# Optimization experiments

Hardware: AMD Instinct MI355X
Metric: run time of the kernel (lower is better)

## Reference

```python
import jax, jax.numpy as jnp
import numpy as np

N_COMP = 48
RES = 300
N_FEAT = 27
N_PTS = 1_000_000


def _sample_plane(plane, gx, gy):
    # plane: [C, H, W]; gx, gy: [N] grid coords in [-1, 1]; bilinear, align_corners=True
    C, H, W = plane.shape
    x = (gx + 1.0) * 0.5 * (W - 1)
    y = (gy + 1.0) * 0.5 * (H - 1)
    x0f = jnp.floor(x)
    y0f = jnp.floor(y)
    wx = x - x0f
    wy = y - y0f
    x0 = jnp.clip(x0f, 0, W - 1).astype(jnp.int32)
    y0 = jnp.clip(y0f, 0, H - 1).astype(jnp.int32)
    x1 = jnp.clip(x0 + 1, 0, W - 1)
    y1 = jnp.clip(y0 + 1, 0, H - 1)
    v00 = plane[:, y0, x0]  # [C, N]
    v01 = plane[:, y0, x1]
    v10 = plane[:, y1, x0]
    v11 = plane[:, y1, x1]
    return (1.0 - wy) * ((1.0 - wx) * v00 + wx * v01) + wy * ((1.0 - wx) * v10 + wx * v11)


def _sample_line(line, gy):
    # line: [C, R] (width dim of size 1 squeezed; grid x == 0 -> column 0); gy: [N]
    C, R = line.shape
    y = (gy + 1.0) * 0.5 * (R - 1)
    y0f = jnp.floor(y)
    wy = y - y0f
    y0 = jnp.clip(y0f, 0, R - 1).astype(jnp.int32)
    y1 = jnp.clip(y0 + 1, 0, R - 1)
    return (1.0 - wy) * line[:, y0] + wy * line[:, y1]  # [C, N]


def setup_inputs():
    key = jax.random.key(0)
    k0, k1, k2, k3 = jax.random.split(key, 4)
    xyz = jax.random.uniform(k0, (N_PTS, 3), jnp.float32) * 2.0 - 1.0
    planes = 0.1 * jax.random.uniform(k1, (3, N_COMP, RES, RES), jnp.float32)
    lines = 0.1 * jax.random.uniform(k2, (3, N_COMP, RES, 1), jnp.float32)
    basis_W = jax.random.normal(k3, (N_FEAT, 3 * N_COMP), jnp.float32) / jnp.sqrt(3.0 * N_COMP)
    return {"xyz_sampled": xyz, "planes": planes, "lines": lines, "basis_W": basis_W}


def reference(xyz_sampled, planes, lines, basis_W):
    # plane i samples (x=xyz[:,a], y=xyz[:,b]) with (a,b) per torch's xyz[..., [2,1]/[2,0]/[1,0]]
    PLANE_AX = ((2, 1), (2, 0), (1, 0))
    pf, lf = [], []
    for i in range(3):
        a, b = PLANE_AX[i]
        pf.append(_sample_plane(planes[i], xyz_sampled[:, a], xyz_sampled[:, b]))
        lf.append(_sample_line(lines[i, :, :, 0], xyz_sampled[:, i]))
    pf = jnp.concatenate(pf, axis=0)  # [3C, N]
    lf = jnp.concatenate(lf, axis=0)  # [3C, N]
    # basis_mat: Linear(3C -> n_features, bias=False) applied to (pf*lf).T
    return (pf * lf).T @ basis_W.T  # [N, n_features]
```

## Files before the change

kernel.cpp:

```cpp
#include <hip/hip_runtime.h>

namespace {

constexpr int NCOMP = 48;
constexpr int RESN  = 300;
constexpr int NFEAT = 27;
constexpr int NPTS  = 1000000;
constexpr int CCTOT = 3 * NCOMP;
constexpr int GRID1 = 32;
constexpr int NBUCKET = GRID1 * GRID1 * GRID1;

typedef _Float16 half_t;
typedef __attribute__((ext_vector_type(8))) _Float16 half8;
typedef __attribute__((ext_vector_type(2))) _Float16 half2_t;
typedef __attribute__((ext_vector_type(8))) short          short8;
typedef __attribute__((ext_vector_type(4))) unsigned int   uint4_t;
typedef __attribute__((ext_vector_type(4))) float          floatx4;

__device__ __forceinline__ unsigned short f32_to_bf16(float x) {
    unsigned u = __float_as_uint(x);
    u += 0x7fffu + ((u >> 16) & 1u);
    return (unsigned short)(u >> 16);
}

__device__ __forceinline__ half2_t bc_h2(float x) {
    union { float f; half2_t h; } u; u.f = x; return u.h;
}
__device__ __forceinline__ float h2_bc(half2_t h) {
    union { float f; half2_t h; } u; u.h = h; return u.f;
}

constexpr int SH_STRIDE = 48;

constexpr int LT_PAD = 64;

constexpr int TP_TOTAL  = 3 * RESN * RESN;
constexpr int TP_BLOCKS = (TP_TOTAL + 255) / 256;
constexpr int LINES_TOT = 3 * RESN;
constexpr int WT_TOT    = NFEAT * CCTOT;
constexpr int WFRAG_TOT = 3 * 2 * 2 * 64 * 8;
constexpr int SU_TOTAL  = LINES_TOT + WT_TOT + WFRAG_TOT + LT_PAD;
constexpr int SU_BLOCKS = (SU_TOTAL + 255) / 256;
constexpr int HB_BLOCKS = (NPTS + 255) / 256;

__device__ __forceinline__ int cell_of(float q) {
    float t = (q + 1.0f) * (0.5f * (float)GRID1);
    int c = (int)t;
    return min(max(c, 0), GRID1 - 1);
}
__device__ __forceinline__ int key_of(float q0, float q1, float q2) {
    return (cell_of(q0) * GRID1 + cell_of(q1)) * GRID1 + cell_of(q2);
}

__global__ __launch_bounds__(256) void fused_front_k(
    const float* __restrict__ planes, const float* __restrict__ lines,
    const float* __restrict__ W, const float* __restrict__ xyz,
    half_t* __restrict__ pt, half_t* __restrict__ lt,
    float* __restrict__ wt, unsigned short* __restrict__ wfrag,
    int* __restrict__ hist) {
    int b = blockIdx.x;
    if (b < TP_BLOCKS) {
        int idx = b * 256 + threadIdx.x;
        if (idx >= TP_TOTAL) return;
        int i   = idx / (RESN * RESN);
        int rem = idx - i * (RESN * RESN);
        const float* s = planes + (size_t)i * NCOMP * RESN * RESN + rem;
        half8* d = (half8*)(pt + (size_t)idx * NCOMP);
#pragma unroll
        for (int g = 0; g < NCOMP / 8; ++g) {
            half8 h;
#pragma unroll
            for (int k = 0; k < 8; ++k)
                h[k] = (half_t)s[(size_t)(g * 8 + k) * (RESN * RESN)];
            d[g] = h;
        }
        return;
    }
    if (b < TP_BLOCKS + SU_BLOCKS) {
        int idx = (b - TP_BLOCKS) * 256 + threadIdx.x;
        if (idx < LINES_TOT) {
            int i = idx / RESN;
            int y = idx - i * RESN;
            const float* s = lines + (size_t)i * NCOMP * RESN + y;
            half8* d = (half8*)(lt + (size_t)idx * NCOMP);
#pragma unroll
            for (int g = 0; g < NCOMP / 8; ++g) {
                half8 h;
#pragma unroll
                for (int k = 0; k < 8; ++k)
                    h[k] = (half_t)s[(size_t)(g * 8 + k) * RESN];
                d[g] = h;
            }
            return;
        }
        idx -= LINES_TOT;
        if (idx < WT_TOT) {
            int f  = idx / CCTOT;
            int cc = idx - f * CCTOT;
            wt[(size_t)cc * NFEAT + f] = W[idx];
            return;
        }
        idx -= WT_TOT;
        if (idx < WFRAG_TOT) {
            int j    = idx & 7;
            int lane = (idx >> 3) & 63;
            int nn   = (idx >> 9) & 1;
            int kb   = (idx >> 10) & 1;
            int md   = idx >> 11;
            int f  = nn * 16 + (lane & 15);
            int kk = kb * 32 + ((lane >> 4) << 3) + j;
            float vf = 0.0f;
            if (f < NFEAT && kk < NCOMP)
                vf = W[(size_t)f * CCTOT + md * NCOMP + kk];
            wfrag[idx] = f32_to_bf16(vf);
            return;
        }
        idx -= WFRAG_TOT;
        if (idx < LT_PAD) lt[(size_t)3 * RESN * NCOMP + idx] = (half_t)0.f;
        return;
    }
    int p = (b - TP_BLOCKS - SU_BLOCKS) * 256 + threadIdx.x;
    if (p >= NPTS || !hist) return;
    float q0 = xyz[3 * (size_t)p + 0];
    float q1 = xyz[3 * (size_t)p + 1];
    float q2 = xyz[3 * (size_t)p + 2];
    atomicAdd(&hist[key_of(q0, q1, q2)], 1);
}


__global__ __launch_bounds__(1024) void scan_k(const int* __restrict__ hist,
                                               int* __restrict__ start) {
    __shared__ int part[1024];
    int t = threadIdx.x;
    int base = t * (NBUCKET / 1024);
    int s = 0;
#pragma unroll 4
    for (int j = 0; j < NBUCKET / 1024; ++j) s += hist[base + j];
    part[t] = s;
    __syncthreads();
    for (int off = 1; off < 1024; off <<= 1) {
        int v = (t >= off) ? part[t - off] : 0;
        __syncthreads();
        part[t] += v;
        __syncthreads();
    }
    int run = (t == 0) ? 0 : part[t - 1];
    for (int j = 0; j < NBUCKET / 1024; ++j) {
        start[base + j] = run;
        run += hist[base + j];
    }
}

__global__ __launch_bounds__(256) void scatter_k(const float* __restrict__ xyz,
                                                 int* __restrict__ start,
                                                 float4* __restrict__ xyzs) {
    int p = blockIdx.x * blockDim.x + threadIdx.x;
    if (p >= NPTS) return;
    float q0 = xyz[3 * (size_t)p + 0];
    float q1 = xyz[3 * (size_t)p + 1];
    float q2 = xyz[3 * (size_t)p + 2];
    int slot = atomicAdd(&start[key_of(q0, q1, q2)], 1);
    float4 v;
    v.x = q0; v.y = q1; v.z = q2; v.w = __int_as_float(p);
    xyzs[slot] = v;
}


__device__ __forceinline__ void mfma_phase(const unsigned short* __restrict__ shw,
                                           int r, int q,
                                           short8 blo0, short8 blo1,
                                           short8 bhi0, short8 bhi1,
                                           floatx4 acc[4][2]) {
    const short8 z8 = {0, 0, 0, 0, 0, 0, 0, 0};
#pragma unroll
    for (int m = 0; m < 4; ++m) {
        const unsigned short* rb = shw + (size_t)(m * 16 + r) * SH_STRIDE;
        short8 alo = *(const short8*)(rb + q * 8);
        short8 ahl = *(const short8*)(rb + 32 + (q & 1) * 8);
        short8 ahi = (q < 2) ? ahl : z8;
        acc[m][0] = __builtin_amdgcn_mfma_f32_16x16x32_bf16(alo, blo0, acc[m][0], 0, 0, 0);
        acc[m][0] = __builtin_amdgcn_mfma_f32_16x16x32_bf16(ahi, bhi0, acc[m][0], 0, 0, 0);
        acc[m][1] = __builtin_amdgcn_mfma_f32_16x16x32_bf16(alo, blo1, acc[m][1], 0, 0, 0);
        acc[m][1] = __builtin_amdgcn_mfma_f32_16x16x32_bf16(ahi, bhi1, acc[m][1], 0, 0, 0);
    }
}

constexpr int MAIN_BLK = 128;
constexpr int MAIN_NWG = (NPTS + MAIN_BLK - 1) / MAIN_BLK;

__device__ __forceinline__ int swz_main(int orig) {
    constexpr int Q = MAIN_NWG / 8, R = MAIN_NWG % 8;
    int x = orig & 7, p = orig >> 3;
    return (x < R ? x * (Q + 1) : R * (Q + 1) + (x - R) * Q) + p;
}

__global__ __launch_bounds__(MAIN_BLK, 4) void tensor_vm_mfma_kernel(
    const float4* __restrict__ xyzs,
    const half_t* __restrict__ pt,
    const half_t* __restrict__ lt,
    const unsigned short* __restrict__ wfrag,
    float* __restrict__ out) {
    __shared__ unsigned short sh[2][64][SH_STRIDE];
    __shared__ float          sp[2][64][8];

    const int bid = swz_main(blockIdx.x);
    const int tid = threadIdx.x;
    const int w  = tid >> 6;
    const int ln = tid & 63;
    const int r  = ln & 15;
    const int q  = ln >> 4;
    const int gidx = bid * MAIN_BLK + tid;
    const int i = min(gidx, NPTS - 1);
    float4 v = xyzs[i];
    const int permInt = __float_as_int(v.w);

    floatx4 acc[4][2];
    const floatx4 z = {0.f, 0.f, 0.f, 0.f};
#pragma unroll
    for (int m = 0; m < 4; ++m) { acc[m][0] = z; acc[m][1] = z; }

    constexpr size_t PSZ = (size_t)RESN * RESN * NCOMP;
    constexpr size_t LSZ = (size_t)RESN * NCOMP;

    const unsigned short* shw = &sh[w][0][0];

    const float gxs[3] = {v.z, v.z, v.y};
    const float gys[3] = {v.y, v.x, v.x};
    const float gls[3] = {v.x, v.y, v.z};

#pragma unroll
    for (int md = 0; md < 3; ++md) {
        const unsigned short* wfb = wfrag + (size_t)md * 2048 + (size_t)ln * 8;
        short8 blo0 = *(const short8*)(wfb);
        short8 blo1 = *(const short8*)(wfb + 512);
        short8 bhi0 = *(const short8*)(wfb + 1024);
        short8 bhi1 = *(const short8*)(wfb + 1536);

        {
            float x = (gxs[md] + 1.0f) * 0.5f * (float)(RESN - 1);
            float y = (gys[md] + 1.0f) * 0.5f * (float)(RESN - 1);
            float l = (gls[md] + 1.0f) * 0.5f * (float)(RESN - 1);
            float x0f = floorf(x), y0f = floorf(y), l0f = floorf(l);
            float wx = x - x0f, wy = y - y0f, wl = l - l0f;
            int x0 = max(0, min((int)x0f, RESN - 1));
            int y0 = max(0, min((int)y0f, RESN - 1));
            int l0 = max(0, min((int)l0f, RESN - 1));
            int y1 = min(y0 + 1, RESN - 1);
            int off0 = (y0 * RESN + x0) * NCOMP * 2;
            int off1 = (y1 * RESN + x0) * NCOMP * 2;
            int offL = l0 * NCOMP * 2;
            half_t hx = (half_t)wx, hy = (half_t)wy, hl = (half_t)wl;
            half2_t wx2 = {hx, hx}, wy2 = {hy, hy}, wl2 = {hl, hl};
            float4 A, B;
            A.x = __int_as_float(off0); A.y = __int_as_float(off1);
            A.z = __int_as_float(offL); A.w = h2_bc(wx2);
            B.x = h2_bc(wy2); B.y = h2_bc(wl2); B.z = 0.f; B.w = 0.f;
            *(float4*)&sp[w][ln][0] = A;
            *(float4*)&sp[w][ln][4] = B;
        }
        __builtin_amdgcn_sched_barrier(0);

        const char* pmd = (const char*)(pt + md * PSZ);
        const char* lmd = (const char*)(lt + md * LSZ);
#pragma unroll
        for (int it = 0; it < 6; ++it) {
            unsigned pair = (unsigned)(it * 64 + ln);
            unsigned p = (pair * 10923u) >> 16;
            unsigned s = pair - p * 6u;
            float4 A = *(const float4*)&sp[w][p][0];
            float4 B = *(const float4*)&sp[w][p][4];
            int off0 = __float_as_int(A.x);
            int off1 = __float_as_int(A.y);
            int offL = __float_as_int(A.z);
            half2_t wx2 = bc_h2(A.w), wy2 = bc_h2(B.x), wl2 = bc_h2(B.y);
            int so = (int)(s * 16u);
            union H8 { half8 v; half2_t h2[4]; } a, b, c, d, e, f;
            a.v = *(const half8*)(pmd + off0 + so);
            b.v = *(const half8*)(pmd + off0 + 96 + so);
            c.v = *(const half8*)(pmd + off1 + so);
            d.v = *(const half8*)(pmd + off1 + 96 + so);
            e.v = *(const half8*)(lmd + offL + so);
            f.v = *(const half8*)(lmd + offL + 96 + so);
            uint4_t ho;
#pragma unroll
            for (int k = 0; k < 4; ++k) {
                half2_t pa = a.h2[k], pb = b.h2[k], pc = c.h2[k], pd = d.h2[k];
                half2_t px0 = pa + wx2 * (pb - pa);
                half2_t px1 = pc + wx2 * (pd - pc);
                half2_t pv  = px0 + wy2 * (px1 - px0);
                half2_t lv  = e.h2[k] + wl2 * (f.h2[k] - e.h2[k]);
                half2_t pr  = pv * lv;
                float f0 = (float)pr[0], f1 = (float)pr[1];
                unsigned o;
                asm("v_cvt_pk_bf16_f32 %0, %1, %2" : "=v"(o) : "v"(f0), "v"(f1));
                ho[k] = o;
            }
            *(uint4_t*)(&sh[w][p][s * 8u]) = ho;
        }

        asm volatile("s_waitcnt lgkmcnt(0)" ::: "memory");
        __builtin_amdgcn_sched_barrier(0);
        mfma_phase(shw, r, q, blo0, blo1, bhi0, bhi1, acc);
        __builtin_amdgcn_sched_barrier(0);
    }

    const int blockBase = bid * MAIN_BLK + w * 64;
#pragma unroll
    for (int m = 0; m < 4; ++m) {
#pragma unroll
        for (int rr = 0; rr < 4; ++rr) {
            const int pl = m * 16 + q * 4 + rr;
            const int pp = __shfl(permInt, pl);
            if (blockBase + pl < NPTS) {
                float* o = out + (size_t)pp * NFEAT + r;
                o[0] = acc[m][0][rr];
                if (r < NFEAT - 16) o[16] = acc[m][1][rr];
            }
        }
    }
}


__device__ __forceinline__ void accum_mode(float gx, float gy, float gl,
                                           const half_t* __restrict__ pt_i,
                                           const half_t* __restrict__ lt_i,
                                           const float* __restrict__ wt_i,
                                           float* __restrict__ acc) {
    float x = (gx + 1.0f) * 0.5f * (float)(RESN - 1);
    float y = (gy + 1.0f) * 0.5f * (float)(RESN - 1);
    float l = (gl + 1.0f) * 0.5f * (float)(RESN - 1);
    float x0f = floorf(x), y0f = floorf(y), l0f = floorf(l);
    float wx = x - x0f, wy = y - y0f, wl = l - l0f;
    int x0 = (int)x0f; x0 = max(0, min(x0, RESN - 1));
    int y0 = (int)y0f; y0 = max(0, min(y0, RESN - 1));
    int l0 = (int)l0f; l0 = max(0, min(l0, RESN - 1));
    int x1 = min(x0 + 1, RESN - 1);
    int y1 = min(y0 + 1, RESN - 1);
    int l1 = min(l0 + 1, RESN - 1);
    float w00 = (1.0f - wy) * (1.0f - wx);
    float w01 = (1.0f - wy) * wx;
    float w10 = wy * (1.0f - wx);
    float w11 = wy * wx;
    float wl0 = 1.0f - wl;
    float wl1 = wl;
    const half8* p00 = (const half8*)(pt_i + ((size_t)y0 * RESN + x0) * NCOMP);
    const half8* p01 = (const half8*)(pt_i + ((size_t)y0 * RESN + x1) * NCOMP);
    const half8* p10 = (const half8*)(pt_i + ((size_t)y1 * RESN + x0) * NCOMP);
    const half8* p11 = (const half8*)(pt_i + ((size_t)y1 * RESN + x1) * NCOMP);
    const half8* L0  = (const half8*)(lt_i + (size_t)l0 * NCOMP);
    const half8* L1  = (const half8*)(lt_i + (size_t)l1 * NCOMP);
#pragma unroll 2
    for (int g = 0; g < NCOMP / 8; ++g) {
        half8 a = p00[g], b = p01[g], c = p10[g], d = p11[g];
        half8 e0 = L0[g], e1 = L1[g];
#pragma unroll
        for (int j = 0; j < 8; ++j) {
            float pv = w00 * (float)a[j] + w01 * (float)b[j]
                     + w10 * (float)c[j] + w11 * (float)d[j];
            float lv = wl0 * (float)e0[j] + wl1 * (float)e1[j];
            float pr = pv * lv;
            const float* wrow = wt_i + (size_t)(8 * g + j) * NFEAT;
#pragma unroll
            for (int f = 0; f < NFEAT; ++f)
                acc[f] += pr * wrow[f];
        }
    }
}

__global__ __launch_bounds__(256) void tensor_vm_kernel(
    const float* __restrict__ xyz,
    const half_t* __restrict__ pt,
    const half_t* __restrict__ lt,
    const float* __restrict__ wt,
    float* __restrict__ out) {
    int p = blockIdx.x * blockDim.x + threadIdx.x;
    if (p >= NPTS) return;
    float q0 = xyz[3 * (size_t)p + 0];
    float q1 = xyz[3 * (size_t)p + 1];
    float q2 = xyz[3 * (size_t)p + 2];
    float acc[NFEAT];
#pragma unroll
    for (int f = 0; f < NFEAT; ++f) acc[f] = 0.0f;
    constexpr size_t PSZ = (size_t)RESN * RESN * NCOMP;
    constexpr size_t LSZ = (size_t)RESN * NCOMP;
    constexpr int    WSZ = NCOMP * NFEAT;
    accum_mode(q2, q1, q0, pt,           lt,           wt,           acc);
    accum_mode(q2, q0, q1, pt + PSZ,     lt + LSZ,     wt + WSZ,     acc);
    accum_mode(q1, q0, q2, pt + 2 * PSZ, lt + 2 * LSZ, wt + 2 * WSZ, acc);
    float* o = out + (size_t)p * NFEAT;
#pragma unroll
    for (int f = 0; f < NFEAT; ++f) o[f] = acc[f];
}

__global__ __launch_bounds__(256) void tensor_vm_naive_kernel(
    const float* __restrict__ xyz,
    const float* __restrict__ planes,
    const float* __restrict__ lines,
    const float* __restrict__ W,
    float* __restrict__ out) {
    int p = blockIdx.x * blockDim.x + threadIdx.x;
    if (p >= NPTS) return;
    float q[3];
    q[0] = xyz[3 * (size_t)p + 0];
    q[1] = xyz[3 * (size_t)p + 1];
    q[2] = xyz[3 * (size_t)p + 2];
    float acc[NFEAT];
    for (int f = 0; f < NFEAT; ++f) acc[f] = 0.0f;
    const int AX[3] = {2, 2, 1};
    const int BX[3] = {1, 0, 0};
    for (int i = 0; i < 3; ++i) {
        float gx = q[AX[i]], gy = q[BX[i]], gl = q[i];
        float x = (gx + 1.0f) * 0.5f * (float)(RESN - 1);
        float y = (gy + 1.0f) * 0.5f * (float)(RESN - 1);
        float l = (gl + 1.0f) * 0.5f * (float)(RESN - 1);
        float x0f = floorf(x), y0f = floorf(y), l0f = floorf(l);
        float wx = x - x0f, wy = y - y0f, wl = l - l0f;
        int x0 = max(0, min((int)x0f, RESN - 1));
        int y0 = max(0, min((int)y0f, RESN - 1));
        int l0 = max(0, min((int)l0f, RESN - 1));
        int x1 = min(x0 + 1, RESN - 1);
        int y1 = min(y0 + 1, RESN - 1);
        int l1 = min(l0 + 1, RESN - 1);
        float w00 = (1.0f - wy) * (1.0f - wx);
        float w01 = (1.0f - wy) * wx;
        float w10 = wy * (1.0f - wx);
        float w11 = wy * wx;
        const float* pl = planes + (size_t)i * NCOMP * RESN * RESN;
        const float* ln = lines + (size_t)i * NCOMP * RESN;
        for (int c = 0; c < NCOMP; ++c) {
            const float* plc = pl + (size_t)c * RESN * RESN;
            float v00 = plc[(size_t)y0 * RESN + x0];
            float v01 = plc[(size_t)y0 * RESN + x1];
            float v10 = plc[(size_t)y1 * RESN + x0];
            float v11 = plc[(size_t)y1 * RESN + x1];
            float pv = w00 * v00 + w01 * v01 + w10 * v10 + w11 * v11;
            float lv = (1.0f - wl) * ln[(size_t)c * RESN + l0] + wl * ln[(size_t)c * RESN + l1];
            float pr = pv * lv;
            int cc = i * NCOMP + c;
            for (int f = 0; f < NFEAT; ++f)
                acc[f] += pr * W[(size_t)f * CCTOT + cc];
        }
    }
    float* o = out + (size_t)p * NFEAT;
    for (int f = 0; f < NFEAT; ++f) o[f] = acc[f];
}

}

extern "C" void kernel_launch(void* const* d_in, const int* in_sizes, int n_in,
                              void* d_out, int out_size, void* d_ws, size_t ws_size,
                              hipStream_t stream) {
    (void)in_sizes; (void)n_in; (void)out_size;
    const float* xyz    = (const float*)d_in[0];
    const float* planes = (const float*)d_in[1];
    const float* lines  = (const float*)d_in[2];
    const float* W      = (const float*)d_in[3];
    float* out = (float*)d_out;

    constexpr size_t PT_HALVES   = (size_t)3 * RESN * RESN * NCOMP;
    constexpr size_t LT_HALVES   = (size_t)3 * RESN * NCOMP + LT_PAD;
    constexpr size_t WT_FLOATS   = (size_t)CCTOT * NFEAT;

    constexpr size_t WT_BYTES    = WT_FLOATS * sizeof(float);
    constexpr size_t WFRAG_BYTES = (size_t)WFRAG_TOT * 2;
    constexpr size_t PT_BYTES    = PT_HALVES * sizeof(half_t);
    constexpr size_t LT_BYTES    = LT_HALVES * sizeof(half_t);
    constexpr size_t HIST_BYTES  = (size_t)NBUCKET * sizeof(int);
    constexpr size_t XYZS_BYTES  = (size_t)NPTS * sizeof(float4);
    constexpr size_t NEED_PLAIN  = WT_BYTES + WFRAG_BYTES + PT_BYTES + LT_BYTES;
    constexpr size_t NEED_SORT   = NEED_PLAIN + 2 * HIST_BYTES + XYZS_BYTES;

    if (ws_size >= NEED_PLAIN) {
        float*          wt    = (float*)d_ws;
        unsigned short* wfrag = (unsigned short*)((char*)d_ws + WT_BYTES);
        half_t*         pt    = (half_t*)((char*)d_ws + WT_BYTES + WFRAG_BYTES);
        half_t*         lt    = (half_t*)((char*)d_ws + WT_BYTES + WFRAG_BYTES + PT_BYTES);
        if (ws_size >= NEED_SORT) {
            int*    hist  = (int*)((char*)d_ws + NEED_PLAIN);
            int*    start = (int*)((char*)d_ws + NEED_PLAIN + HIST_BYTES);
            float4* xyzs  = (float4*)((char*)d_ws + NEED_PLAIN + 2 * HIST_BYTES);
            hipMemsetAsync(hist, 0, HIST_BYTES, stream);
            fused_front_k<<<TP_BLOCKS + SU_BLOCKS + HB_BLOCKS, 256, 0, stream>>>(
                planes, lines, W, xyz, pt, lt, wt, wfrag, hist);
            scan_k<<<1, 1024, 0, stream>>>(hist, start);
            scatter_k<<<(NPTS + 255) / 256, 256, 0, stream>>>(xyz, start, xyzs);
            tensor_vm_mfma_kernel<<<MAIN_NWG, MAIN_BLK, 0, stream>>>(
                xyzs, pt, lt, wfrag, out);
        } else {
            fused_front_k<<<TP_BLOCKS + SU_BLOCKS, 256, 0, stream>>>(
                planes, lines, W, xyz, pt, lt, wt, wfrag, nullptr);
            tensor_vm_kernel<<<(NPTS + 255) / 256, 256, 0, stream>>>(xyz, pt, lt, wt, out);
        }
    } else {
        tensor_vm_naive_kernel<<<(NPTS + 255) / 256, 256, 0, stream>>>(xyz, planes, lines, W, out);
    }
}
```

Baseline: 401.8 us.

## Drop spatial bucket sort and XCD swizzle; read xyz directly in MFMA kernel

Removes the histogram, scan and scatter passes that sorted points into 32^3 spatial buckets, along with the XCD-aware block swizzle. The MFMA kernel now reads the raw xyz input in original order and writes output rows directly, with no permutation shuffle. This saves the memset, the atomics, a single-block scan and an extra pass over the points. The cost is that, with uniformly random points, neighbouring threads gather from scattered plane texels, so cache locality on the roughly 26 MB fp16 plane table is lost.

Measured after the change: 359.6 us. 1.12x faster.

```diff
diff --git a/kernel.cpp b/kernel.cpp
--- a/kernel.cpp
+++ b/kernel.cpp
@@ -7,8 +7,6 @@
 constexpr int NFEAT = 27;
 constexpr int NPTS  = 1000000;
 constexpr int CCTOT = 3 * NCOMP;
-constexpr int GRID1 = 32;
-constexpr int NBUCKET = GRID1 * GRID1 * GRID1;
 
 typedef _Float16 half_t;
 typedef __attribute__((ext_vector_type(8))) _Float16 half8;
@@ -41,23 +39,12 @@
 constexpr int WFRAG_TOT = 3 * 2 * 2 * 64 * 8;
 constexpr int SU_TOTAL  = LINES_TOT + WT_TOT + WFRAG_TOT + LT_PAD;
 constexpr int SU_BLOCKS = (SU_TOTAL + 255) / 256;
-constexpr int HB_BLOCKS = (NPTS + 255) / 256;
-
-__device__ __forceinline__ int cell_of(float q) {
-    float t = (q + 1.0f) * (0.5f * (float)GRID1);
-    int c = (int)t;
-    return min(max(c, 0), GRID1 - 1);
-}
-__device__ __forceinline__ int key_of(float q0, float q1, float q2) {
-    return (cell_of(q0) * GRID1 + cell_of(q1)) * GRID1 + cell_of(q2);
-}
 
 __global__ __launch_bounds__(256) void fused_front_k(
     const float* __restrict__ planes, const float* __restrict__ lines,
-    const float* __restrict__ W, const float* __restrict__ xyz,
+    const float* __restrict__ W,
     half_t* __restrict__ pt, half_t* __restrict__ lt,
-    float* __restrict__ wt, unsigned short* __restrict__ wfrag,
-    int* __restrict__ hist) {
+    float* __restrict__ wt, unsigned short* __restrict__ wfrag) {
     int b = blockIdx.x;
     if (b < TP_BLOCKS) {
         int idx = b * 256 + threadIdx.x;
@@ -76,93 +63,46 @@
         }
         return;
     }
-    if (b < TP_BLOCKS + SU_BLOCKS) {
-        int idx = (b - TP_BLOCKS) * 256 + threadIdx.x;
-        if (idx < LINES_TOT) {
-            int i = idx / RESN;
-            int y = idx - i * RESN;
-            const float* s = lines + (size_t)i * NCOMP * RESN + y;
-            half8* d = (half8*)(lt + (size_t)idx * NCOMP);
-#pragma unroll
-            for (int g = 0; g < NCOMP / 8; ++g) {
-                half8 h;
-#pragma unroll
-                for (int k = 0; k < 8; ++k)
-                    h[k] = (half_t)s[(size_t)(g * 8 + k) * RESN];
-                d[g] = h;
-            }
-            return;
-        }
-        idx -= LINES_TOT;
-        if (idx < WT_TOT) {
-            int f  = idx / CCTOT;
-            int cc = idx - f * CCTOT;
-            wt[(size_t)cc * NFEAT + f] = W[idx];
-            return;
-        }
-        idx -= WT_TOT;
-        if (idx < WFRAG_TOT) {
-            int j    = idx & 7;
-            int lane = (idx >> 3) & 63;
-            int nn   = (idx >> 9) & 1;
-            int kb   = (idx >> 10) & 1;
-            int md   = idx >> 11;
-            int f  = nn * 16 + (lane & 15);
-            int kk = kb * 32 + ((lane >> 4) << 3) + j;
-            float vf = 0.0f;
-            if (f < NFEAT && kk < NCOMP)
-                vf = W[(size_t)f * CCTOT + md * NCOMP + kk];
-            wfrag[idx] = f32_to_bf16(vf);
-            return;
-        }
-        idx -= WFRAG_TOT;
-        if (idx < LT_PAD) lt[(size_t)3 * RESN * NCOMP + idx] = (half_t)0.f;
+    int idx = (b - TP_BLOCKS) * 256 + threadIdx.x;
+    if (idx < LINES_TOT) {
+        int i = idx / RESN;
+        int y = idx - i * RESN;
+        const float* s = lines + (size_t)i * NCOMP * RESN + y;
+        half8* d = (half8*)(lt + (size_t)idx * NCOMP);
+#pragma unroll
+        for (int g = 0; g < NCOMP / 8; ++g) {
+            half8 h;
+#pragma unroll
+            for (int k = 0; k < 8; ++k)
+                h[k] = (half_t)s[(size_t)(g * 8 + k) * RESN];
+            d[g] = h;
+        }
         return;
     }
-    int p = (b - TP_BLOCKS - SU_BLOCKS) * 256 + threadIdx.x;
-    if (p >= NPTS || !hist) return;
-    float q0 = xyz[3 * (size_t)p + 0];
-    float q1 = xyz[3 * (size_t)p + 1];
-    float q2 = xyz[3 * (size_t)p + 2];
-    atomicAdd(&hist[key_of(q0, q1, q2)], 1);
-}
-
-
-__global__ __launch_bounds__(1024) void scan_k(const int* __restrict__ hist,
-                                               int* __restrict__ start) {
-    __shared__ int part[1024];
-    int t = threadIdx.x;
-    int base = t * (NBUCKET / 1024);
-    int s = 0;
-#pragma unroll 4
-    for (int j = 0; j < NBUCKET / 1024; ++j) s += hist[base + j];
-    part[t] = s;
-    __syncthreads();
-    for (int off = 1; off < 1024; off <<= 1) {
-        int v = (t >= off) ? part[t - off] : 0;
-        __syncthreads();
-        part[t] += v;
-        __syncthreads();
-    }
-    int run = (t == 0) ? 0 : part[t - 1];
-    for (int j = 0; j < NBUCKET / 1024; ++j) {
-        start[base + j] = run;
-        run += hist[base + j];
-    }
-}
-
-__global__ __launch_bounds__(256) void scatter_k(const float* __restrict__ xyz,
-                                                 int* __restrict__ start,
-                                                 float4* __restrict__ xyzs) {
-    int p = blockIdx.x * blockDim.x + threadIdx.x;
-    if (p >= NPTS) return;
-    float q0 = xyz[3 * (size_t)p + 0];
-    float q1 = xyz[3 * (size_t)p + 1];
-    float q2 = xyz[3 * (size_t)p + 2];
-    int slot = atomicAdd(&start[key_of(q0, q1, q2)], 1);
-    float4 v;
-    v.x = q0; v.y = q1; v.z = q2; v.w = __int_as_float(p);
-    xyzs[slot] = v;
+    idx -= LINES_TOT;
+    if (idx < WT_TOT) {
+        int f  = idx / CCTOT;
+        int cc = idx - f * CCTOT;
+        wt[(size_t)cc * NFEAT + f] = W[idx];
+        return;
+    }
+    idx -= WT_TOT;
+    if (idx < WFRAG_TOT) {
+        int j    = idx & 7;
+        int lane = (idx >> 3) & 63;
+        int nn   = (idx >> 9) & 1;
+        int kb   = (idx >> 10) & 1;
+        int md   = idx >> 11;
+        int f  = nn * 16 + (lane & 15);
+        int kk = kb * 32 + ((lane >> 4) << 3) + j;
+        float vf = 0.0f;
+        if (f < NFEAT && kk < NCOMP)
+            vf = W[(size_t)f * CCTOT + md * NCOMP + kk];
+        wfrag[idx] = f32_to_bf16(vf);
+        return;
+    }
+    idx -= WFRAG_TOT;
+    if (idx < LT_PAD) lt[(size_t)3 * RESN * NCOMP + idx] = (half_t)0.f;
 }
 
 
@@ -188,14 +128,8 @@
 constexpr int MAIN_BLK = 128;
 constexpr int MAIN_NWG = (NPTS + MAIN_BLK - 1) / MAIN_BLK;
 
-__device__ __forceinline__ int swz_main(int orig) {
-    constexpr int Q = MAIN_NWG / 8, R = MAIN_NWG % 8;
-    int x = orig & 7, p = orig >> 3;
-    return (x < R ? x * (Q + 1) : R * (Q + 1) + (x - R) * Q) + p;
-}
-
 __global__ __launch_bounds__(MAIN_BLK, 4) void tensor_vm_mfma_kernel(
-    const float4* __restrict__ xyzs,
+    const float* __restrict__ xyz,
     const half_t* __restrict__ pt,
     const half_t* __restrict__ lt,
     const unsigned short* __restrict__ wfrag,
@@ -203,7 +137,7 @@
     __shared__ unsigned short sh[2][64][SH_STRIDE];
     __shared__ float          sp[2][64][8];
 
-    const int bid = swz_main(blockIdx.x);
+    const int bid = blockIdx.x;
     const int tid = threadIdx.x;
     const int w  = tid >> 6;
     const int ln = tid & 63;
@@ -211,8 +145,9 @@
     const int q  = ln >> 4;
     const int gidx = bid * MAIN_BLK + tid;
     const int i = min(gidx, NPTS - 1);
-    float4 v = xyzs[i];
-    const int permInt = __float_as_int(v.w);
+    const float q0v = xyz[3 * (size_t)i + 0];
+    const float q1v = xyz[3 * (size_t)i + 1];
+    const float q2v = xyz[3 * (size_t)i + 2];
 
     floatx4 acc[4][2];
     const floatx4 z = {0.f, 0.f, 0.f, 0.f};
@@ -224,9 +159,9 @@
 
     const unsigned short* shw = &sh[w][0][0];
 
-    const float gxs[3] = {v.z, v.z, v.y};
-    const float gys[3] = {v.y, v.x, v.x};
-    const float gls[3] = {v.x, v.y, v.z};
+    const float gxs[3] = {q2v, q2v, q1v};
+    const float gys[3] = {q1v, q0v, q0v};
+    const float gls[3] = {q0v, q1v, q2v};
 
 #pragma unroll
     for (int md = 0; md < 3; ++md) {
@@ -309,9 +244,8 @@
     for (int m = 0; m < 4; ++m) {
 #pragma unroll
         for (int rr = 0; rr < 4; ++rr) {
-            const int pl = m * 16 + q * 4 + rr;
-            const int pp = __shfl(permInt, pl);
-            if (blockBase + pl < NPTS) {
+            const int pp = blockBase + m * 16 + q * 4 + rr;
+            if (pp < NPTS) {
                 float* o = out + (size_t)pp * NFEAT + r;
                 o[0] = acc[m][0][rr];
                 if (r < NFEAT - 16) o[16] = acc[m][1][rr];
@@ -465,32 +399,17 @@
     constexpr size_t WFRAG_BYTES = (size_t)WFRAG_TOT * 2;
     constexpr size_t PT_BYTES    = PT_HALVES * sizeof(half_t);
     constexpr size_t LT_BYTES    = LT_HALVES * sizeof(half_t);
-    constexpr size_t HIST_BYTES  = (size_t)NBUCKET * sizeof(int);
-    constexpr size_t XYZS_BYTES  = (size_t)NPTS * sizeof(float4);
     constexpr size_t NEED_PLAIN  = WT_BYTES + WFRAG_BYTES + PT_BYTES + LT_BYTES;
-    constexpr size_t NEED_SORT   = NEED_PLAIN + 2 * HIST_BYTES + XYZS_BYTES;
 
     if (ws_size >= NEED_PLAIN) {
         float*          wt    = (float*)d_ws;
         unsigned short* wfrag = (unsigned short*)((char*)d_ws + WT_BYTES);
         half_t*         pt    = (half_t*)((char*)d_ws + WT_BYTES + WFRAG_BYTES);
         half_t*         lt    = (half_t*)((char*)d_ws + WT_BYTES + WFRAG_BYTES + PT_BYTES);
-        if (ws_size >= NEED_SORT) {
-            int*    hist  = (int*)((char*)d_ws + NEED_PLAIN);
-            int*    start = (int*)((char*)d_ws + NEED_PLAIN + HIST_BYTES);
-            float4* xyzs  = (float4*)((char*)d_ws + NEED_PLAIN + 2 * HIST_BYTES);
-            hipMemsetAsync(hist, 0, HIST_BYTES, stream);
-            fused_front_k<<<TP_BLOCKS + SU_BLOCKS + HB_BLOCKS, 256, 0, stream>>>(
-                planes, lines, W, xyz, pt, lt, wt, wfrag, hist);
-            scan_k<<<1, 1024, 0, stream>>>(hist, start);
-            scatter_k<<<(NPTS + 255) / 256, 256, 0, stream>>>(xyz, start, xyzs);
-            tensor_vm_mfma_kernel<<<MAIN_NWG, MAIN_BLK, 0, stream>>>(
-                xyzs, pt, lt, wfrag, out);
-        } else {
-            fused_front_k<<<TP_BLOCKS + SU_BLOCKS, 256, 0, stream>>>(
-                planes, lines, W, xyz, pt, lt, wt, wfrag, nullptr);
-            tensor_vm_kernel<<<(NPTS + 255) / 256, 256, 0, stream>>>(xyz, pt, lt, wt, out);
-        }
+        fused_front_k<<<TP_BLOCKS + SU_BLOCKS, 256, 0, stream>>>(
+            planes, lines, W, pt, lt, wt, wfrag);
+        tensor_vm_mfma_kernel<<<MAIN_NWG, MAIN_BLK, 0, stream>>>(
+            xyz, pt, lt, wfrag, out);
     } else {
         tensor_vm_naive_kernel<<<(NPTS + 255) / 256, 256, 0, stream>>>(xyz, planes, lines, W, out);
     }
```
